# Performance work log

Measured on AMD Instinct MI355X. Metric: run time of the kernel, lower is better.

Reference implementation:

```python
import jax, jax.numpy as jnp
import numpy as np

NEG_SLOPE = 0.2
F_OUT = 64


def setup_inputs() -> dict:
    key = jax.random.key(0)
    k1, k2, k3 = jax.random.split(key, 3)
    N, F_IN = 8192, 256
    h = jax.random.normal(k1, (N, F_IN), dtype=jnp.float32)
    adj = jnp.ones((N, N), dtype=jnp.bool_)  # unused by the original forward
    # xavier-uniform-ish init scale
    W = jax.random.uniform(k2, (F_IN, F_OUT), dtype=jnp.float32,
                           minval=-1.0, maxval=1.0) * np.sqrt(6.0 / (F_IN + F_OUT))
    a = jax.random.uniform(k3, (2 * F_OUT, 1), dtype=jnp.float32,
                           minval=-1.0, maxval=1.0) * np.sqrt(6.0 / (2 * F_OUT + 1))
    return {"h": h, "adj": adj, "W": W, "a": a}


def reference(h, adj, W, a):
    # Wh: [N, F_OUT]
    Wh = h @ W
    # The torch code materializes an [N*N, F] repeat to compute what is just
    # a broadcast add of two projected score vectors:
    # e[i, j] = leakyrelu(Wh[i] @ a1 + Wh[j] @ a2)
    s1 = Wh @ a[:F_OUT]   # [N, 1]
    s2 = Wh @ a[F_OUT:]   # [N, 1]
    e = s1 + s2.T         # [N, N]
    e = jnp.where(e >= 0, e, NEG_SLOPE * e)  # LeakyReLU(0.2)
    attention = jax.nn.softmax(e, axis=1)    # note: adj is NOT used (matches source)
    return attention @ Wh                    # [N, F_OUT]
```

## Files before the change

### kernel.cpp

```cpp
#include <hip/hip_runtime.h>
#include <math.h>

#define GN 8192
#define GF 64
#define GFIN 256
#define NEG 0.2f
#define NFINE 256
#define FCH 32

#define OFF_WH   0
#define OFF_S1   (GN*GF)
#define OFF_S2   (OFF_S1 + GN)
#define OFF_ZS   (OFF_S2 + GN)
#define OFF_IDX  (OFF_ZS + GN)
#define OFF_OFA  (OFF_IDX + GN)
#define OFF_OFB  (OFF_OFA + NFINE*GF)
#define OFF_OSA  (OFF_OFB + NFINE*GF)
#define OFF_OSB  (OFF_OSA + NFINE)

__global__ __launch_bounds__(512) void k_wh(const float* __restrict__ h,
        const float* __restrict__ W, const float* __restrict__ a,
        float* __restrict__ wsf) {
    float* Wh = wsf + OFF_WH;
    float* s1 = wsf + OFF_S1;
    float* s2 = wsf + OFF_S2;
    __shared__ float Wl[GFIN*GF];
    int t = threadIdx.x, b = blockIdx.x;
    int lane = t & 63;
    const float4* W4 = (const float4*)W;
    float4* Wl4 = (float4*)Wl;
    #pragma unroll
    for (int m = 0; m < 8; ++m) Wl4[t + m*512] = W4[t + m*512];
    __syncthreads();
    int wid = __builtin_amdgcn_readfirstlane(t >> 6);
    int row0 = b*32 + wid*4;
    const float* hrow = h + (size_t)row0 * GFIN;
    float acc[4] = {0.f,0.f,0.f,0.f};
    #pragma unroll 8
    for (int k = 0; k < GFIN; ++k) {
        float wv = Wl[k*GF + lane];
        #pragma unroll
        for (int q = 0; q < 4; ++q) acc[q] += hrow[q*GFIN + k] * wv;
    }
    float a1 = a[lane], a2 = a[GF + lane];
    #pragma unroll
    for (int q = 0; q < 4; ++q) {
        int row = row0 + q;
        Wh[(size_t)row*GF + lane] = acc[q];
        float v1 = acc[q]*a1, v2 = acc[q]*a2;
        #pragma unroll
        for (int o = 32; o > 0; o >>= 1) { v1 += __shfl_xor(v1, o); v2 += __shfl_xor(v2, o); }
        if (lane == 0) { s1[row] = v1; s2[row] = v2; }
    }
}

__global__ __launch_bounds__(512) void k_rank(float* __restrict__ wsf) {
    __shared__ float zl[GN];
    const float* s2 = wsf + OFF_S2;
    float* zs = wsf + OFF_ZS;
    int* idx = (int*)(wsf + OFF_IDX);
    int t = threadIdx.x, b = blockIdx.x;
    const float4* s4 = (const float4*)s2;
    float4* z4 = (float4*)zl;
    for (int m = t; m < GN/4; m += 512) z4[m] = s4[m];
    __syncthreads();
    int jl = t >> 4, sl = t & 15;
    int j = b*32 + jl;
    float zj = zl[j];
    int cnt = 0;
    #pragma unroll 4
    for (int i = 0; i < GN/64; ++i) {
        int m4 = i*16 + sl;
        float4 v = z4[m4];
        int mb = m4*4;
        cnt += (v.x < zj) || (v.x == zj && mb   < j);
        cnt += (v.y < zj) || (v.y == zj && mb+1 < j);
        cnt += (v.z < zj) || (v.z == zj && mb+2 < j);
        cnt += (v.w < zj) || (v.w == zj && mb+3 < j);
    }
    cnt += __shfl_xor(cnt, 1);
    cnt += __shfl_xor(cnt, 2);
    cnt += __shfl_xor(cnt, 4);
    cnt += __shfl_xor(cnt, 8);
    if (sl == 0) { zs[cnt] = zj; idx[cnt] = j; }
}

__global__ __launch_bounds__(256) void k_colscan(float* __restrict__ wsf) {
    __shared__ float stg[NFINE];
    __shared__ float wred[4];
    const float* Wh = wsf + OFF_WH;
    const float* zs = wsf + OFF_ZS;
    const int* idx = (const int*)(wsf + OFF_IDX);
    float* ofA = wsf + OFF_OFA;
    float* ofB = wsf + OFF_OFB;
    float* osA = wsf + OFF_OSA;
    float* osB = wsf + OFF_OSB;
    int c = blockIdx.x;
    int t = threadIdx.x, lane = t & 63, wid = t >> 6;
    float Z = zs[GN-1];
    float fA = 0.f, fB = 0.f;
    #pragma unroll 8
    for (int q = 0; q < FCH; ++q) {
        int r = t*FCH + q;
        float d = zs[r] - Z;
        float tA = __expf(d);
        float tB = __expf(NEG*d);
        float w = (c < 64) ? Wh[(size_t)idx[r]*GF + c] : 1.0f;
        fA += tA*w; fB += tB*w;
    }
    {
        float ws = fB;
        #pragma unroll
        for (int o = 1; o < 64; o <<= 1) { float y = __shfl_up(ws, o); if (lane >= o) ws += y; }
        if (lane == 63) wred[wid] = ws;
        __syncthreads();
        float blkoff = 0.f;
        #pragma unroll
        for (int w2 = 0; w2 < 4; ++w2) { float x = wred[w2]; if (w2 < wid) blkoff += x; }
        float exB = blkoff + ws - fB;
        if (c < 64) ofB[t*GF + c] = exB; else osB[t] = exB;
    }
    __syncthreads();
    stg[t] = fA;
    __syncthreads();
    {
        int rt = NFINE-1-t;
        float vA = stg[rt];
        float ws = vA;
        #pragma unroll
        for (int o = 1; o < 64; o <<= 1) { float y = __shfl_up(ws, o); if (lane >= o) ws += y; }
        __syncthreads();
        if (lane == 63) wred[wid] = ws;
        __syncthreads();
        float blkoff = 0.f;
        #pragma unroll
        for (int w2 = 0; w2 < 4; ++w2) { float x = wred[w2]; if (w2 < wid) blkoff += x; }
        float exA = blkoff + ws - vA;
        if (c < 64) ofA[rt*GF + c] = exA; else osA[rt] = exA;
    }
}

__global__ __launch_bounds__(256) void k_out(const float* __restrict__ wsf,
        float* __restrict__ out) {
    const float* Wh = wsf + OFF_WH;
    const float* s1 = wsf + OFF_S1;
    const float* zs = wsf + OFF_ZS;
    const int* idx = (const int*)(wsf + OFF_IDX);
    const float* ofA = wsf + OFF_OFA;
    const float* ofB = wsf + OFF_OFB;
    const float* osA = wsf + OFF_OSA;
    const float* osB = wsf + OFF_OSB;
    int t = threadIdx.x;
    int wid = t >> 6, lane = t & 63;
    int i = blockIdx.x*4 + wid;
    float s1i = s1[i];
    float Z = zs[GN-1];
    float g = s1i + Z;
    float m = (g >= 0.f) ? g : NEG*g;
    float aA = __expf(g - m);
    float aB = __expf(NEG*g - m);
    float tgt = -s1i;
    int lo = 0, hi = GN;
    #pragma unroll
    for (int it = 0; it < 13; ++it) {
        int mid = (lo + hi) >> 1;
        if (zs[mid] < tgt) lo = mid + 1; else hi = mid;
    }
    int k = lo;
    int fc = __builtin_amdgcn_readfirstlane(min(k >> 5, NFINE-1));
    float va = ofA[fc*GF + lane];
    float vb = ofB[fc*GF + lane];
    float sa = osA[fc], pb = osB[fc];
    #pragma unroll 8
    for (int q = 0; q < FCH; ++q) {
        int r = fc*FCH + q;
        float zr = zs[r];
        int ir = idx[r];
        float w = Wh[(size_t)ir*GF + lane];
        float d = zr - Z;
        if (r >= k) { float tA = __expf(d);     va += tA*w; sa += tA; }
        else        { float tB = __expf(NEG*d); vb += tB*w; pb += tB; }
    }
    out[(size_t)i*GF + lane] = (aA*va + aB*vb) / (aA*sa + aB*pb);
}

extern "C" void kernel_launch(void* const* d_in, const int* in_sizes, int n_in,
                              void* d_out, int out_size, void* d_ws, size_t ws_size,
                              hipStream_t stream) {
    const float* h = (const float*)d_in[0];
    const float* W = (const float*)d_in[2];
    const float* a = (const float*)d_in[3];
    float* wsf = (float*)d_ws;
    float* out = (float*)d_out;

    hipLaunchKernelGGL(k_wh,      dim3(GN/32), dim3(512), 0, stream, h, W, a, wsf);
    hipLaunchKernelGGL(k_rank,    dim3(GN/32), dim3(512), 0, stream, wsf);
    hipLaunchKernelGGL(k_colscan, dim3(65),    dim3(256), 0, stream, wsf);
    hipLaunchKernelGGL(k_out,     dim3(GN/4),  dim3(256), 0, stream, wsf, out);
}
```

Baseline: 69.48 us.

## Fuse per-chunk exp-weighted sums into rank kernel via atomics; transpose W in LDS

The per-fine-chunk exponential-weighted sums of Wh, previously computed in the 65-block colscan kernel by gathering sorted rows, are now accumulated in the rank kernel with global atomics once each row's rank is known. Each rank block also computes the global max of s2 itself. The colscan kernel becomes a pure prefix scan over the precomputed chunk sums. Separately, k_wh stores W transposed and XOR-swizzled in LDS so each lane reads float4s. The trade-off is atomic contention, a zeroing pass in k_wh, and non-deterministic float summation order.

Measured after the change: 70.99 us. +2.2%, slower.

```diff
diff --git a/kernel.cpp b/kernel.cpp
--- a/kernel.cpp
+++ b/kernel.cpp
@@ -13,10 +13,15 @@
 #define OFF_S2   (OFF_S1 + GN)
 #define OFF_ZS   (OFF_S2 + GN)
 #define OFF_IDX  (OFF_ZS + GN)
-#define OFF_OFA  (OFF_IDX + GN)
+#define OFF_FA   (OFF_IDX + GN)
+#define OFF_FB   (OFF_FA + NFINE*GF)
+#define OFF_FSA  (OFF_FB + NFINE*GF)
+#define OFF_FSB  (OFF_FSA + NFINE)
+#define OFF_OFA  (OFF_FSB + NFINE)
 #define OFF_OFB  (OFF_OFA + NFINE*GF)
 #define OFF_OSA  (OFF_OFB + NFINE*GF)
 #define OFF_OSB  (OFF_OSA + NFINE)
+#define ZERO_CNT (2*NFINE*GF + 2*NFINE)
 
 __global__ __launch_bounds__(512) void k_wh(const float* __restrict__ h,
         const float* __restrict__ W, const float* __restrict__ a,
@@ -24,23 +29,42 @@
     float* Wh = wsf + OFF_WH;
     float* s1 = wsf + OFF_S1;
     float* s2 = wsf + OFF_S2;
-    __shared__ float Wl[GFIN*GF];
+    __shared__ float WlT[GF*GFIN];
     int t = threadIdx.x, b = blockIdx.x;
+    int zm = b*512 + t;
+    if (zm < ZERO_CNT) wsf[OFF_FA + zm] = 0.f;
     int lane = t & 63;
     const float4* W4 = (const float4*)W;
-    float4* Wl4 = (float4*)Wl;
-    #pragma unroll
-    for (int m = 0; m < 8; ++m) Wl4[t + m*512] = W4[t + m*512];
+    #pragma unroll
+    for (int m = 0; m < 8; ++m) {
+        int g = t + m*512;
+        float4 v = W4[g];
+        int k = g >> 4;
+        int c0 = (g & 15) * 4;
+        WlT[(c0  )*GFIN + (k ^ (((c0  )&7)<<2))] = v.x;
+        WlT[(c0+1)*GFIN + (k ^ (((c0+1)&7)<<2))] = v.y;
+        WlT[(c0+2)*GFIN + (k ^ (((c0+2)&7)<<2))] = v.z;
+        WlT[(c0+3)*GFIN + (k ^ (((c0+3)&7)<<2))] = v.w;
+    }
     __syncthreads();
     int wid = __builtin_amdgcn_readfirstlane(t >> 6);
     int row0 = b*32 + wid*4;
     const float* hrow = h + (size_t)row0 * GFIN;
     float acc[4] = {0.f,0.f,0.f,0.f};
+    const float4* WlT4 = (const float4*)WlT;
+    int cbase = lane * (GFIN/4);
+    int sw = lane & 7;
     #pragma unroll 8
-    for (int k = 0; k < GFIN; ++k) {
-        float wv = Wl[k*GF + lane];
-        #pragma unroll
-        for (int q = 0; q < 4; ++q) acc[q] += hrow[q*GFIN + k] * wv;
+    for (int k4 = 0; k4 < GFIN/4; ++k4) {
+        float4 wv = WlT4[cbase + (k4 ^ sw)];
+        int kk = k4*4;
+        #pragma unroll
+        for (int q = 0; q < 4; ++q) {
+            acc[q] += hrow[q*GFIN + kk  ] * wv.x;
+            acc[q] += hrow[q*GFIN + kk+1] * wv.y;
+            acc[q] += hrow[q*GFIN + kk+2] * wv.z;
+            acc[q] += hrow[q*GFIN + kk+3] * wv.w;
+        }
     }
     float a1 = a[lane], a2 = a[GF + lane];
     #pragma unroll
@@ -54,16 +78,34 @@
     }
 }
 
-__global__ __launch_bounds__(512) void k_rank(float* __restrict__ wsf) {
+__global__ __launch_bounds__(512) void k_rank(const float* __restrict__ Whg,
+        float* __restrict__ wsf) {
     __shared__ float zl[GN];
+    __shared__ int rl[32];
+    __shared__ float redm[8];
     const float* s2 = wsf + OFF_S2;
     float* zs = wsf + OFF_ZS;
     int* idx = (int*)(wsf + OFF_IDX);
+    float* fineA = wsf + OFF_FA;
+    float* fineB = wsf + OFF_FB;
+    float* fSA = wsf + OFF_FSA;
+    float* fSB = wsf + OFF_FSB;
     int t = threadIdx.x, b = blockIdx.x;
+    int lane = t & 63, wid = t >> 6;
     const float4* s4 = (const float4*)s2;
     float4* z4 = (float4*)zl;
-    for (int m = t; m < GN/4; m += 512) z4[m] = s4[m];
-    __syncthreads();
+    float mx = -1e30f;
+    for (int m = t; m < GN/4; m += 512) {
+        float4 v = s4[m]; z4[m] = v;
+        mx = fmaxf(fmaxf(mx, v.x), fmaxf(fmaxf(v.y, v.z), v.w));
+    }
+    #pragma unroll
+    for (int o = 32; o > 0; o >>= 1) mx = fmaxf(mx, __shfl_xor(mx, o));
+    if (lane == 0) redm[wid] = mx;
+    __syncthreads();
+    float Z = redm[0];
+    #pragma unroll
+    for (int w2 = 1; w2 < 8; ++w2) Z = fmaxf(Z, redm[w2]);
     int jl = t >> 4, sl = t & 15;
     int j = b*32 + jl;
     float zj = zl[j];
@@ -82,32 +124,40 @@
     cnt += __shfl_xor(cnt, 2);
     cnt += __shfl_xor(cnt, 4);
     cnt += __shfl_xor(cnt, 8);
-    if (sl == 0) { zs[cnt] = zj; idx[cnt] = j; }
-}
-
-__global__ __launch_bounds__(256) void k_colscan(float* __restrict__ wsf) {
+    if (sl == 0) { zs[cnt] = zj; idx[cnt] = j; rl[jl] = cnt; }
+    __syncthreads();
+    #pragma unroll
+    for (int q = 0; q < 4; ++q) {
+        int jj = wid*4 + q;
+        int jg = b*32 + jj;
+        int r = rl[jj];
+        float d = zl[jg] - Z;
+        float tA = __expf(d);
+        float tB = __expf(NEG*d);
+        float w = Whg[(size_t)jg*GF + lane];
+        int fc = r >> 5;
+        atomicAdd(&fineA[fc*GF + lane], tA*w);
+        atomicAdd(&fineB[fc*GF + lane], tB*w);
+        if (lane == 0) atomicAdd(&fSA[fc], tA);
+        if (lane == 1) atomicAdd(&fSB[fc], tB);
+    }
+}
+
+__global__ __launch_bounds__(256) void k_scan(float* __restrict__ wsf) {
     __shared__ float stg[NFINE];
     __shared__ float wred[4];
-    const float* Wh = wsf + OFF_WH;
-    const float* zs = wsf + OFF_ZS;
-    const int* idx = (const int*)(wsf + OFF_IDX);
+    const float* fineA = wsf + OFF_FA;
+    const float* fineB = wsf + OFF_FB;
+    const float* fSA = wsf + OFF_FSA;
+    const float* fSB = wsf + OFF_FSB;
     float* ofA = wsf + OFF_OFA;
     float* ofB = wsf + OFF_OFB;
     float* osA = wsf + OFF_OSA;
     float* osB = wsf + OFF_OSB;
     int c = blockIdx.x;
     int t = threadIdx.x, lane = t & 63, wid = t >> 6;
-    float Z = zs[GN-1];
-    float fA = 0.f, fB = 0.f;
-    #pragma unroll 8
-    for (int q = 0; q < FCH; ++q) {
-        int r = t*FCH + q;
-        float d = zs[r] - Z;
-        float tA = __expf(d);
-        float tB = __expf(NEG*d);
-        float w = (c < 64) ? Wh[(size_t)idx[r]*GF + c] : 1.0f;
-        fA += tA*w; fB += tB*w;
-    }
+    float fA = (c < 64) ? fineA[t*GF + c] : fSA[t];
+    float fB = (c < 64) ? fineB[t*GF + c] : fSB[t];
     {
         float ws = fB;
         #pragma unroll
@@ -193,8 +243,8 @@
     float* wsf = (float*)d_ws;
     float* out = (float*)d_out;
 
-    hipLaunchKernelGGL(k_wh,      dim3(GN/32), dim3(512), 0, stream, h, W, a, wsf);
-    hipLaunchKernelGGL(k_rank,    dim3(GN/32), dim3(512), 0, stream, wsf);
-    hipLaunchKernelGGL(k_colscan, dim3(65),    dim3(256), 0, stream, wsf);
-    hipLaunchKernelGGL(k_out,     dim3(GN/4),  dim3(256), 0, stream, wsf, out);
-}
+    hipLaunchKernelGGL(k_wh,   dim3(GN/32), dim3(512), 0, stream, h, W, a, wsf);
+    hipLaunchKernelGGL(k_rank, dim3(GN/32), dim3(512), 0, stream, wsf + OFF_WH, wsf);
+    hipLaunchKernelGGL(k_scan, dim3(65),    dim3(256), 0, stream, wsf);
+    hipLaunchKernelGGL(k_out,  dim3(GN/4),  dim3(256), 0, stream, wsf, out);
+}
```
